# Optimization experiments

Measured on AMD Instinct MI355X. Metric: run time of the kernel, lower is better.

Reference implementation:

```python
import jax, jax.numpy as jnp
import numpy as np

DIM = 1024
NUM_HEADS = 16
HEAD_DIM = DIM // NUM_HEADS


def setup_inputs() -> dict:
    key = jax.random.key(0)
    k1, k2, k3 = jax.random.split(key, 3)
    x = jax.random.normal(k1, (4, 1024, DIM), dtype=jnp.float32)
    # match nn.Linear init scale roughly: small weights
    Wqkv = jax.random.normal(k2, (3 * DIM, DIM), dtype=jnp.float32) * (1.0 / np.sqrt(DIM))
    Wproj = jax.random.normal(k3, (DIM, DIM), dtype=jnp.float32) * (1.0 / np.sqrt(DIM))
    bproj = jnp.zeros((DIM,), dtype=jnp.float32)
    return {"x": x, "Wqkv": Wqkv, "Wproj": Wproj, "bproj": bproj}


def reference(x, Wqkv, Wproj, bproj):
    bsz, tsz, chans = x.shape
    # fused QKV projection (qkv_bias=False): [B,T,3C]
    qkv = jnp.einsum("btc,oc->bto", x, Wqkv)
    qkv = qkv.reshape(bsz, tsz, 3, NUM_HEADS, HEAD_DIM)
    q = qkv[:, :, 0].transpose(0, 2, 1, 3)  # [B,H,T,D]
    k = qkv[:, :, 1].transpose(0, 2, 1, 3)
    v = qkv[:, :, 2].transpose(0, 2, 1, 3)
    scale = 1.0 / np.sqrt(HEAD_DIM)
    logits = jnp.einsum("bhqd,bhkd->bhqk", q, k) * scale  # [B,H,T,T]
    attn = jax.nn.softmax(logits, axis=-1)
    out = jnp.einsum("bhqk,bhkd->bhqd", attn, v)  # [B,H,T,D]
    out = out.transpose(0, 2, 1, 3).reshape(bsz, tsz, chans)
    return jnp.einsum("btc,oc->bto", out, Wproj) + bproj
```

## Files before the change

kernel.cpp:

```cpp
#include <hip/hip_runtime.h>
#include <hip/hip_bf16.h>

typedef __attribute__((ext_vector_type(8))) short bfrag8;
typedef __attribute__((ext_vector_type(4))) short bfrag4;
typedef __attribute__((ext_vector_type(4))) float floatx4;

typedef unsigned short ushort_t;
typedef unsigned int uint_t;
typedef unsigned long long u64_t;

static __device__ __forceinline__ uint_t pk_bf16(float a, float b) {
    union { __hip_bfloat162 h; uint_t u; } cv;
    cv.h = __float22bfloat162_rn(make_float2(a, b));
    return cv.u;
}

#if __has_builtin(__builtin_amdgcn_mfma_f32_16x16x16_bf16)
static __device__ __forceinline__ floatx4 mfma16(bfrag4 a, bfrag4 b, floatx4 c) {
    return __builtin_amdgcn_mfma_f32_16x16x16_bf16(a, b, c, 0, 0, 0);
}
#elif __has_builtin(__builtin_amdgcn_mfma_f32_16x16x16bf16_1k)
static __device__ __forceinline__ floatx4 mfma16(bfrag4 a, bfrag4 b, floatx4 c) {
    return __builtin_amdgcn_mfma_f32_16x16x16bf16_1k(a, b, c, 0, 0, 0);
}
#else
static __device__ __forceinline__ floatx4 mfma16(bfrag4 a, bfrag4 b, floatx4 c) {
    bfrag8 az = {a[0], 0, a[1], 0, a[2], 0, a[3], 0};
    bfrag8 bz = {b[0], 0, b[1], 0, b[2], 0, b[3], 0};
    return __builtin_amdgcn_mfma_f32_16x16x32_bf16(az, bz, c, 0, 0, 0);
}
#endif

static __device__ __forceinline__ void gl_lds16(const ushort_t* g, ushort_t* l) {
    __builtin_amdgcn_global_load_lds(
        (const __attribute__((address_space(1))) void*)g,
        (__attribute__((address_space(3))) void*)l, 16, 0, 0);
}

__global__ __launch_bounds__(256)
void cvt_all(const float* __restrict__ x, const float* __restrict__ wqkv,
             const float* __restrict__ wproj, ushort_t* __restrict__ xb,
             ushort_t* __restrict__ wqkvb, ushort_t* __restrict__ wprojb) {
    int blk = blockIdx.x;
    const float* src; ushort_t* dst; int base;
    if (blk < 4096)      { src = x;     dst = xb;     base = blk; }
    else if (blk < 7168) { src = wqkv;  dst = wqkvb;  base = blk - 4096; }
    else                 { src = wproj; dst = wprojb; base = blk - 7168; }
    int i = (base * 256 + threadIdx.x) * 4;
    float4 f = *(const float4*)(src + i);
    uint_t lo = pk_bf16(f.x, f.y);
    uint_t hi = pk_bf16(f.z, f.w);
    uint2 u = {lo, hi};
    *(uint2*)(dst + i) = u;
}

__global__ __launch_bounds__(256, 3)
void qkv_gemm(const ushort_t* __restrict__ A, const ushort_t* __restrict__ B,
              ushort_t* __restrict__ qp, ushort_t* __restrict__ kp,
              ushort_t* __restrict__ vTp) {
    const int K = 1024;
    __shared__ ushort_t As[128 * 64];
    __shared__ ushort_t Bs[128 * 64];
    int tid = threadIdx.x;
    int wave = __builtin_amdgcn_readfirstlane(tid >> 6);
    int lane = tid & 63;
    int quad = lane >> 4, l16 = lane & 15;
    int wm = (wave >> 1) * 64, wn = (wave & 1) * 64;
    int m0 = blockIdx.y * 128, n0 = blockIdx.x * 128;

    int rl = lane >> 3;
    int gc = (lane & 7) ^ rl;

    floatx4 acc[4][4] = {};

    const ushort_t* Ag = A + (size_t)m0 * K;
    const ushort_t* Bg = B + (size_t)n0 * K;

    for (int k0 = 0; k0 < K; k0 += 64) {
        __syncthreads();
#pragma unroll
        for (int i = 0; i < 4; i++) {
            int row = wave * 32 + i * 8 + rl;
            gl_lds16(Ag + (size_t)row * K + k0 + gc * 8, &As[(wave * 32 + i * 8) * 64]);
            gl_lds16(Bg + (size_t)row * K + k0 + gc * 8, &Bs[(wave * 32 + i * 8) * 64]);
        }
        __syncthreads();
#pragma unroll
        for (int ks = 0; ks < 2; ks++) {
            bfrag8 af[4], bf[4];
#pragma unroll
            for (int mt = 0; mt < 4; mt++) {
                int r = wm + mt * 16 + l16;
                af[mt] = *(const bfrag8*)&As[r * 64 + ((4 * ks + quad) ^ (r & 7)) * 8];
            }
#pragma unroll
            for (int nt = 0; nt < 4; nt++) {
                int r = wn + nt * 16 + l16;
                bf[nt] = *(const bfrag8*)&Bs[r * 64 + ((4 * ks + quad) ^ (r & 7)) * 8];
            }
#pragma unroll
            for (int mt = 0; mt < 4; mt++)
#pragma unroll
                for (int nt = 0; nt < 4; nt++)
                    acc[mt][nt] = __builtin_amdgcn_mfma_f32_16x16x32_bf16(
                        af[mt], bf[nt], acc[mt][nt], 0, 0, 0);
        }
    }

    int s = n0 >> 10;
    if (s < 2) {
        ushort_t* dst = (s == 0) ? qp : kp;
        float scl = (s == 0) ? 0.125f : 1.0f;
#pragma unroll
        for (int mt = 0; mt < 4; mt++) {
#pragma unroll
            for (int nt = 0; nt < 4; nt++) {
                int o = (n0 & 1023) + wn + nt * 16 + l16;
                int h = o >> 6, d = o & 63;
                uint_t p01 = pk_bf16(acc[mt][nt][0] * scl, acc[mt][nt][1] * scl);
                uint_t p23 = pk_bf16(acc[mt][nt][2] * scl, acc[mt][nt][3] * scl);
                ushort_t pv[4] = {(ushort_t)p01, (ushort_t)(p01 >> 16),
                                  (ushort_t)p23, (ushort_t)(p23 >> 16)};
#pragma unroll
                for (int r = 0; r < 4; r++) {
                    int t = m0 + wm + mt * 16 + quad * 4 + r;
                    int b = t >> 10, tt = t & 1023;
                    dst[((size_t)(b * 16 + h) * 1024 + tt) * 64 + d] = pv[r];
                }
            }
        }
    } else {
#pragma unroll
        for (int mt = 0; mt < 4; mt++) {
            int t = m0 + wm + mt * 16 + quad * 4;
            int b = t >> 10, tt = t & 1023;
#pragma unroll
            for (int nt = 0; nt < 4; nt++) {
                int o = (n0 & 1023) + wn + nt * 16 + l16;
                int h = o >> 6, d = o & 63;
                uint_t p01 = pk_bf16(acc[mt][nt][0], acc[mt][nt][1]);
                uint_t p23 = pk_bf16(acc[mt][nt][2], acc[mt][nt][3]);
                u64_t pk = ((u64_t)p23 << 32) | p01;
                *(u64_t*)&vTp[((size_t)(b * 16 + h) * 64 + d) * 1024 + tt] = pk;
            }
        }
    }
}

__global__ __launch_bounds__(256, 4)
void attn_kernel(const ushort_t* __restrict__ q, const ushort_t* __restrict__ k,
                 const ushort_t* __restrict__ vT, ushort_t* __restrict__ out) {
    int id = blockIdx.x;
    int bh = (id & 7) + ((id >> 6) << 3);
    int qt = (id >> 3) & 7;
    const ushort_t* qb = q + (size_t)bh * 1024 * 64;
    const ushort_t* kb = k + (size_t)bh * 1024 * 64;
    const ushort_t* vtb = vT + (size_t)bh * 64 * 1024;
    int tid = threadIdx.x;
    int wave = __builtin_amdgcn_readfirstlane(tid >> 6);
    int lane = tid & 63;
    int quad = lane >> 4, l16 = lane & 15;
    int q0 = qt * 128 + wave * 32;

    __shared__ ushort_t Ks[128 * 64];
    __shared__ ushort_t VTs[64 * 132];

    int rl = lane >> 3;
    int gc = (lane & 7) ^ rl;

    bfrag8 qf[2][2];
#pragma unroll
    for (int mt = 0; mt < 2; mt++)
#pragma unroll
        for (int ks = 0; ks < 2; ks++)
            qf[mt][ks] = *(const bfrag8*)&qb[(size_t)(q0 + mt * 16 + l16) * 64 + ks * 32 + quad * 8];

    floatx4 oacc[2][4] = {};
    float li[2] = {0.f, 0.f};

    int vd = tid >> 2;
    int vc = tid & 3;

    for (int kt = 0; kt < 8; kt++) {
        uint4 vv[4];
#pragma unroll
        for (int i = 0; i < 4; i++)
            vv[i] = *(const uint4*)&vtb[(size_t)vd * 1024 + kt * 128 + (vc + i * 4) * 8];
        __syncthreads();
#pragma unroll
        for (int i = 0; i < 4; i++) {
            int row = wave * 32 + i * 8 + rl;
            gl_lds16(kb + (size_t)(kt * 128 + row) * 64 + gc * 8, &Ks[(wave * 32 + i * 8) * 64]);
        }
#pragma unroll
        for (int i = 0; i < 4; i++)
            *(uint4*)&VTs[vd * 132 + (vc + i * 4) * 8] = vv[i];
        __syncthreads();

#pragma unroll
        for (int half = 0; half < 2; half++) {
            floatx4 st[2][4] = {};
#pragma unroll
            for (int ks = 0; ks < 2; ks++) {
                bfrag8 kf[4];
#pragma unroll
                for (int tt = 0; tt < 4; tt++) {
                    int r = (half * 4 + tt) * 16 + l16;
                    kf[tt] = *(const bfrag8*)&Ks[r * 64 + ((4 * ks + quad) ^ (r & 7)) * 8];
                }
#pragma unroll
                for (int mt = 0; mt < 2; mt++)
#pragma unroll
                    for (int tt = 0; tt < 4; tt++)
                        st[mt][tt] = __builtin_amdgcn_mfma_f32_16x16x32_bf16(
                            kf[tt], qf[mt][ks], st[mt][tt], 0, 0, 0);
            }

            bfrag4 pf[2][4];
#pragma unroll
            for (int mt = 0; mt < 2; mt++)
#pragma unroll
                for (int tt = 0; tt < 4; tt++) {
                    float p0 = __expf(st[mt][tt][0]);
                    float p1 = __expf(st[mt][tt][1]);
                    float p2 = __expf(st[mt][tt][2]);
                    float p3 = __expf(st[mt][tt][3]);
                    li[mt] += (p0 + p1) + (p2 + p3);
                    union { uint2 u; bfrag4 f; } pk;
                    pk.u.x = pk_bf16(p0, p1);
                    pk.u.y = pk_bf16(p2, p3);
                    pf[mt][tt] = pk.f;
                }

#pragma unroll
            for (int tt = 0; tt < 4; tt++) {
                int keyoff = (half * 4 + tt) * 16;
                bfrag4 vb[4];
#pragma unroll
                for (int nd = 0; nd < 4; nd++)
                    vb[nd] = *(const bfrag4*)&VTs[(nd * 16 + l16) * 132 + keyoff + quad * 4];
#pragma unroll
                for (int mt = 0; mt < 2; mt++)
#pragma unroll
                    for (int nd = 0; nd < 4; nd++)
                        oacc[mt][nd] = mfma16(pf[mt][tt], vb[nd], oacc[mt][nd]);
            }
        }
    }

    float inv[2][4];
#pragma unroll
    for (int mt = 0; mt < 2; mt++) {
        float s0 = li[mt];
        s0 += __shfl_xor(s0, 16);
        s0 += __shfl_xor(s0, 32);
#pragma unroll
        for (int r = 0; r < 4; r++)
            inv[mt][r] = 1.0f / __shfl(s0, quad * 4 + r);
    }

    int b = bh >> 4, h = bh & 15;
#pragma unroll
    for (int mt = 0; mt < 2; mt++)
#pragma unroll
        for (int nd = 0; nd < 4; nd++) {
            uint_t c01 = pk_bf16(oacc[mt][nd][0] * inv[mt][0], oacc[mt][nd][1] * inv[mt][1]);
            uint_t c23 = pk_bf16(oacc[mt][nd][2] * inv[mt][2], oacc[mt][nd][3] * inv[mt][3]);
            ushort_t pv[4] = {(ushort_t)c01, (ushort_t)(c01 >> 16),
                              (ushort_t)c23, (ushort_t)(c23 >> 16)};
#pragma unroll
            for (int r = 0; r < 4; r++) {
                int t = q0 + mt * 16 + quad * 4 + r;
                int c = h * 64 + nd * 16 + l16;
                out[((size_t)(b * 1024 + t)) * 1024 + c] = pv[r];
            }
        }
}

__global__ __launch_bounds__(256, 2)
void proj_gemm(const ushort_t* __restrict__ A, const ushort_t* __restrict__ B,
               const float* __restrict__ bias, float* __restrict__ out) {
    const int K = 1024;
    __shared__ ushort_t As[64 * 64];
    __shared__ ushort_t Bs[128 * 64];
    int tid = threadIdx.x;
    int wave = __builtin_amdgcn_readfirstlane(tid >> 6);
    int lane = tid & 63;
    int quad = lane >> 4, l16 = lane & 15;
    int wm = (wave >> 1) * 32, wn = (wave & 1) * 64;
    int m0 = blockIdx.y * 64, n0 = blockIdx.x * 128;

    int rl = lane >> 3;
    int gc = (lane & 7) ^ rl;

    floatx4 acc[2][4] = {};

    const ushort_t* Ag = A + (size_t)m0 * K;
    const ushort_t* Bg = B + (size_t)n0 * K;

    for (int k0 = 0; k0 < K; k0 += 64) {
        __syncthreads();
#pragma unroll
        for (int i = 0; i < 2; i++) {
            int row = wave * 16 + i * 8 + rl;
            gl_lds16(Ag + (size_t)row * K + k0 + gc * 8, &As[(wave * 16 + i * 8) * 64]);
        }
#pragma unroll
        for (int i = 0; i < 4; i++) {
            int row = wave * 32 + i * 8 + rl;
            gl_lds16(Bg + (size_t)row * K + k0 + gc * 8, &Bs[(wave * 32 + i * 8) * 64]);
        }
        __syncthreads();
#pragma unroll
        for (int ks = 0; ks < 2; ks++) {
            bfrag8 af[2], bf[4];
#pragma unroll
            for (int mt = 0; mt < 2; mt++) {
                int r = wm + mt * 16 + l16;
                af[mt] = *(const bfrag8*)&As[r * 64 + ((4 * ks + quad) ^ (r & 7)) * 8];
            }
#pragma unroll
            for (int nt = 0; nt < 4; nt++) {
                int r = wn + nt * 16 + l16;
                bf[nt] = *(const bfrag8*)&Bs[r * 64 + ((4 * ks + quad) ^ (r & 7)) * 8];
            }
#pragma unroll
            for (int mt = 0; mt < 2; mt++)
#pragma unroll
                for (int nt = 0; nt < 4; nt++)
                    acc[mt][nt] = __builtin_amdgcn_mfma_f32_16x16x32_bf16(
                        af[mt], bf[nt], acc[mt][nt], 0, 0, 0);
        }
    }

#pragma unroll
    for (int mt = 0; mt < 2; mt++) {
#pragma unroll
        for (int nt = 0; nt < 4; nt++) {
            int o = n0 + wn + nt * 16 + l16;
            float bv = bias[o];
#pragma unroll
            for (int r = 0; r < 4; r++) {
                int t = m0 + wm + mt * 16 + quad * 4 + r;
                out[(size_t)t * 1024 + o] = acc[mt][nt][r] + bv;
            }
        }
    }
}

extern "C" void kernel_launch(void* const* d_in, const int* in_sizes, int n_in,
                              void* d_out, int out_size, void* d_ws, size_t ws_size,
                              hipStream_t stream) {
    const float* x     = (const float*)d_in[0];
    const float* Wqkv  = (const float*)d_in[1];
    const float* Wproj = (const float*)d_in[2];
    const float* bproj = (const float*)d_in[3];
    float* out = (float*)d_out;

    char* ws = (char*)d_ws;
    ushort_t* xb     = (ushort_t*)(ws);
    ushort_t* wqkvb  = (ushort_t*)(ws + ((size_t)8 << 20));
    ushort_t* wprojb = (ushort_t*)(ws + ((size_t)14 << 20));
    ushort_t* qp     = (ushort_t*)(ws + ((size_t)16 << 20));
    ushort_t* kp     = (ushort_t*)(ws + ((size_t)24 << 20));
    ushort_t* vTp    = (ushort_t*)(ws + ((size_t)40 << 20));
    ushort_t* attn   = (ushort_t*)(ws + ((size_t)48 << 20));

    cvt_all<<<8192, 256, 0, stream>>>(x, Wqkv, Wproj, xb, wqkvb, wprojb);
    qkv_gemm<<<dim3(24, 32), 256, 0, stream>>>(xb, wqkvb, qp, kp, vTp);
    attn_kernel<<<512, 256, 0, stream>>>(qp, kp, vTp, attn);
    proj_gemm<<<dim3(8, 64), 256, 0, stream>>>(attn, wprojb, bproj, out);
}
```

Baseline: 192.6 us.

## Register-prefetch next K/V tile and fold log2e into Q scale for exp2

The K tile is now loaded through registers instead of direct global-to-LDS copies, and both the K and V tiles for the next iteration are prefetched into registers while the current tile is being computed. This is meant to hide global memory latency behind the MFMA and softmax work. The Q scale now includes log2(e), so the softmax can call the hardware exp2 instruction directly. Launch bounds drop from 4 to 3 blocks per SU to make room for the extra prefetch registers, which may reduce occupancy.

```diff
diff --git a/kernel.cpp b/kernel.cpp
--- a/kernel.cpp
+++ b/kernel.cpp
@@ -13,6 +13,10 @@
     union { __hip_bfloat162 h; uint_t u; } cv;
     cv.h = __float22bfloat162_rn(make_float2(a, b));
     return cv.u;
+}
+
+static __device__ __forceinline__ float fast_exp2(float x) {
+    return __builtin_amdgcn_exp2f(x);
 }
 
 #if __has_builtin(__builtin_amdgcn_mfma_f32_16x16x16_bf16)
@@ -110,7 +114,7 @@
     int s = n0 >> 10;
     if (s < 2) {
         ushort_t* dst = (s == 0) ? qp : kp;
-        float scl = (s == 0) ? 0.125f : 1.0f;
+        float scl = (s == 0) ? 0.125f * 1.44269504f : 1.0f;
 #pragma unroll
         for (int mt = 0; mt < 4; mt++) {
 #pragma unroll
@@ -147,7 +151,7 @@
     }
 }
 
-__global__ __launch_bounds__(256, 4)
+__global__ __launch_bounds__(256, 3)
 void attn_kernel(const ushort_t* __restrict__ q, const ushort_t* __restrict__ k,
                  const ushort_t* __restrict__ vT, ushort_t* __restrict__ out) {
     int id = blockIdx.x;
@@ -166,7 +170,8 @@
     __shared__ ushort_t VTs[64 * 132];
 
     int rl = lane >> 3;
-    int gc = (lane & 7) ^ rl;
+    int lc = lane & 7;
+    int gc = lc ^ rl;
 
     bfrag8 qf[2][2];
 #pragma unroll
@@ -181,21 +186,31 @@
     int vd = tid >> 2;
     int vc = tid & 3;
 
+    uint4 kv[4], vv[4];
+#pragma unroll
+    for (int i = 0; i < 4; i++) {
+        int row = wave * 32 + i * 8 + rl;
+        kv[i] = *(const uint4*)&kb[(size_t)row * 64 + gc * 8];
+        vv[i] = *(const uint4*)&vtb[(size_t)vd * 1024 + (vc + i * 4) * 8];
+    }
+
     for (int kt = 0; kt < 8; kt++) {
-        uint4 vv[4];
-#pragma unroll
-        for (int i = 0; i < 4; i++)
-            vv[i] = *(const uint4*)&vtb[(size_t)vd * 1024 + kt * 128 + (vc + i * 4) * 8];
         __syncthreads();
 #pragma unroll
         for (int i = 0; i < 4; i++) {
             int row = wave * 32 + i * 8 + rl;
-            gl_lds16(kb + (size_t)(kt * 128 + row) * 64 + gc * 8, &Ks[(wave * 32 + i * 8) * 64]);
-        }
-#pragma unroll
-        for (int i = 0; i < 4; i++)
+            *(uint4*)&Ks[row * 64 + lc * 8] = kv[i];
             *(uint4*)&VTs[vd * 132 + (vc + i * 4) * 8] = vv[i];
-        __syncthreads();
+        }
+        __syncthreads();
+        if (kt < 7) {
+#pragma unroll
+            for (int i = 0; i < 4; i++) {
+                int row = wave * 32 + i * 8 + rl;
+                kv[i] = *(const uint4*)&kb[(size_t)((kt + 1) * 128 + row) * 64 + gc * 8];
+                vv[i] = *(const uint4*)&vtb[(size_t)vd * 1024 + (kt + 1) * 128 + (vc + i * 4) * 8];
+            }
+        }
 
 #pragma unroll
         for (int half = 0; half < 2; half++) {
@@ -221,10 +236,10 @@
             for (int mt = 0; mt < 2; mt++)
 #pragma unroll
                 for (int tt = 0; tt < 4; tt++) {
-                    float p0 = __expf(st[mt][tt][0]);
-                    float p1 = __expf(st[mt][tt][1]);
-                    float p2 = __expf(st[mt][tt][2]);
-                    float p3 = __expf(st[mt][tt][3]);
+                    float p0 = fast_exp2(st[mt][tt][0]);
+                    float p1 = fast_exp2(st[mt][tt][1]);
+                    float p2 = fast_exp2(st[mt][tt][2]);
+                    float p3 = fast_exp2(st[mt][tt][3]);
                     li[mt] += (p0 + p1) + (p2 + p3);
                     union { uint2 u; bfrag4 f; } pk;
                     pk.u.x = pk_bf16(p0, p1);
```

Result: no change. 189.9 us (-1.4%).
